# Performance work log

Hardware: AMD Instinct MI355X
Metric: run time of the kernel (lower is better)

Reference implementation:

```python
import jax, jax.numpy as jnp
import numpy as np

L = 9  # local window size


def local_windows(x, l):
    # x: (n, c, h, w) -> (n, c, l*l, h, w): all l*l shifted views (zero-padded),
    # equivalent to F.unfold(x, kernel=(l,l), stride=1, padding=l//2).
    n, c, h, w = x.shape
    pad = l // 2
    xp = jnp.pad(x, ((0, 0), (0, 0), (pad, pad), (pad, pad)))
    views = [xp[:, :, i:i + h, j:j + w] for i in range(l) for j in range(l)]
    return jnp.stack(views, axis=2)


def setup_inputs() -> dict:
    key = jax.random.key(0)
    k1, k2, k3 = jax.random.split(key, 3)
    n, c, h, w = 2, 128, 64, 64
    ft = jax.random.normal(k1, (n, c, h, w), dtype=jnp.float32)
    fk = jax.random.normal(k2, (n, c, h, w), dtype=jnp.float32)
    # 1x1 conv weight shared between key and query projections: (out_c, in_c)
    W = jax.random.normal(k3, (128, 128), dtype=jnp.float32) * (1.0 / np.sqrt(128))
    return {"ft": ft, "fk": fk, "W": W}


def reference(ft, fk, W):
    # 1x1 conv == channel matmul
    key = jnp.einsum('oi,nihw->nohw', W, ft)    # key from frame t
    query = jnp.einsum('oi,nihw->nohw', W, fk)  # query from frame k
    # f_similar(query, key, L): per-pixel query dotted with L*L local keys
    key_win = local_windows(key, L)             # (n, c, L*L, h, w)
    sim = jnp.einsum('nchw,nckhw->nhwk', query, key_win)  # (n, h, w, L*L)
    weight = jax.nn.softmax(sim, axis=-1)
    # f_weighting(ft, weight, L): weighted sum of L*L local raw-ft vectors
    ft_win = local_windows(ft, L)                # (n, c, L*L, h, w)
    out = jnp.einsum('nckhw,nhwk->nchw', ft_win, weight)
    return out
```

## Files before the change

kernel.cpp:

```cpp
#include <hip/hip_runtime.h>
#include <hip/hip_bf16.h>


#define Hh 64
#define Ww 64
#define Cc 128
#define Nn 2
#define KK 81
#define HW (Hh * Ww)
#define CHW (Cc * HW)
#define P_TOT (Nn * HW)

typedef _Float16 h8 __attribute__((ext_vector_type(8)));
typedef _Float16 h4 __attribute__((ext_vector_type(4)));
typedef _Float16 h2 __attribute__((ext_vector_type(2)));

__device__ __forceinline__ void fma4(float4& a, const float4 b, const float s) {
    a.x += b.x * s; a.y += b.y * s; a.z += b.z * s; a.w += b.w * s;
}

__device__ __forceinline__ float dot8(const h8 a, const h8 b, float acc) {
#if __has_builtin(__builtin_amdgcn_fdot2)
    h2 a0 = {a[0], a[1]}, b0 = {b[0], b[1]};
    h2 a1 = {a[2], a[3]}, b1 = {b[2], b[3]};
    h2 a2 = {a[4], a[5]}, b2 = {b[4], b[5]};
    h2 a3 = {a[6], a[7]}, b3 = {b[6], b[7]};
    acc = __builtin_amdgcn_fdot2(a0, b0, acc, false);
    acc = __builtin_amdgcn_fdot2(a1, b1, acc, false);
    acc = __builtin_amdgcn_fdot2(a2, b2, acc, false);
    acc = __builtin_amdgcn_fdot2(a3, b3, acc, false);
#else
#pragma unroll
    for (int i = 0; i < 8; ++i) acc += (float)a[i] * (float)b[i];
#endif
    return acc;
}

__global__ __launch_bounds__(256) void proj_kernel(const float* __restrict__ ft,
                                                   const float* __restrict__ fk,
                                                   const float* __restrict__ Wm,
                                                   _Float16* __restrict__ Qbuf,
                                                   _Float16* __restrict__ Kbuf,
                                                   _Float16* __restrict__ fth) {
    __shared__ __align__(16) float Wl[32 * 132];
    __shared__ __align__(16) float xkl[128 * 36];
    __shared__ __align__(16) float xql[128 * 36];
    const int t = threadIdx.x;
    const int p0 = blockIdx.x * 32;
    const int nn = p0 >> 12;
    const int gbase = nn * CHW + (p0 & 4095);

    for (int e = t; e < 128 * 32; e += 256) {
        const int c = e >> 5, pl = e & 31;
        xkl[c * 36 + pl] = ft[gbase + c * HW + pl];
        xql[c * 36 + pl] = fk[gbase + c * HW + pl];
    }

    const int po = t & 7;
    const int oo = t >> 3;
    float4 accK[4], accQ[4];
#pragma unroll
    for (int i = 0; i < 4; ++i) { accK[i] = make_float4(0,0,0,0); accQ[i] = make_float4(0,0,0,0); }

    for (int ch = 0; ch < 4; ++ch) {
        for (int e = t; e < 128 * 32; e += 256) {
            const int o = e >> 5, ii = e & 31;
            Wl[ii * 132 + o] = Wm[o * 128 + (ch << 5) + ii];
        }
        __syncthreads();
#pragma unroll 4
        for (int ii = 0; ii < 32; ++ii) {
            const int i = (ch << 5) + ii;
            const float4 w4 = *(const float4*)&Wl[ii * 132 + (oo << 2)];
            const float4 k4 = *(const float4*)&xkl[i * 36 + (po << 2)];
            const float4 q4 = *(const float4*)&xql[i * 36 + (po << 2)];
            fma4(accK[0], k4, w4.x); fma4(accK[1], k4, w4.y);
            fma4(accK[2], k4, w4.z); fma4(accK[3], k4, w4.w);
            fma4(accQ[0], q4, w4.x); fma4(accQ[1], q4, w4.y);
            fma4(accQ[2], q4, w4.z); fma4(accQ[3], q4, w4.w);
        }
        __syncthreads();
    }

    const int pbase = p0 + (po << 2);
    const float kr[4][4] = {
        {accK[0].x, accK[1].x, accK[2].x, accK[3].x},
        {accK[0].y, accK[1].y, accK[2].y, accK[3].y},
        {accK[0].z, accK[1].z, accK[2].z, accK[3].z},
        {accK[0].w, accK[1].w, accK[2].w, accK[3].w}};
    const float qr[4][4] = {
        {accQ[0].x, accQ[1].x, accQ[2].x, accQ[3].x},
        {accQ[0].y, accQ[1].y, accQ[2].y, accQ[3].y},
        {accQ[0].z, accQ[1].z, accQ[2].z, accQ[3].z},
        {accQ[0].w, accQ[1].w, accQ[2].w, accQ[3].w}};
#pragma unroll
    for (int pp = 0; pp < 4; ++pp) {
        const size_t base = (size_t)(pbase + pp) * 128 + (oo << 2);
        h4 kv, qv;
#pragma unroll
        for (int j = 0; j < 4; ++j) { kv[j] = (_Float16)kr[pp][j]; qv[j] = (_Float16)qr[pp][j]; }
        *(h4*)&Kbuf[base] = kv;
        *(h4*)&Qbuf[base] = qv;
    }

#pragma unroll
    for (int pp = 0; pp < 4; ++pp) {
        h4 v;
#pragma unroll
        for (int j = 0; j < 4; ++j)
            v[j] = (_Float16)xkl[((oo << 2) + j) * 36 + (po << 2) + pp];
        *(h4*)&fth[(size_t)(pbase + pp) * 128 + (oo << 2)] = v;
    }
}

__global__ __launch_bounds__(256, 4) void sim_weight_kernel(const _Float16* __restrict__ Qbuf,
                                                            const _Float16* __restrict__ Kbuf,
                                                            const _Float16* __restrict__ fth,
                                                            float* __restrict__ out) {
    __shared__ __align__(16) unsigned char smem[40720];
    _Float16* Ksw  = (_Float16*)smem;
    _Float16* Qsw  = (_Float16*)(smem + 36864);
    _Float16* ftl  = (_Float16*)smem;
    _Float16* simb = (_Float16*)(smem + 39168);
    float*    redM = (float*)(smem + 40464);
    float*    redS = (float*)(smem + 40592);

    const int t  = threadIdx.x;
    const int b  = blockIdx.x;
    const int x0 = (b & 7) << 3;
    const int y  = (b >> 3) & 63;
    const int nn = b >> 9;
    const int pg0 = (nn << 12) + (y << 6) + x0;

#pragma unroll 3
    for (int e = t; e < 144 * 16; e += 256) {
        const int v = e >> 4, ci = e & 15;
        const int gx = x0 + (v & 15) - 4;
        const int gy = y + (v >> 4) - 4;
        h8 val = {0, 0, 0, 0, 0, 0, 0, 0};
        if ((unsigned)gx < 64u && (unsigned)gy < 64u)
            val = *(const h8*)&Kbuf[(size_t)((nn << 12) + (gy << 6) + gx) * 128 + (ci << 3)];
        *(h8*)&Ksw[(v << 7) + ((ci ^ (v & 15)) << 3)] = val;
    }
    if (t < 128) {
        const int v = t >> 4, ci = t & 15;
        *(h8*)&Qsw[(v << 7) + ((ci ^ v) << 3)] =
            *(const h8*)&Qbuf[(size_t)(pg0 + v) * 128 + (ci << 3)];
    }
    __syncthreads();

    const int p = t & 7, kb = t >> 3;
    const bool has2 = (kb + 64 < KK);
    const int k0 = kb, k1 = kb + 32, k2 = has2 ? kb + 64 : kb;
    const int v0 = (k0 / 9) * 16 + p + k0 % 9;
    const int v1 = (k1 / 9) * 16 + p + k1 % 9;
    const int v2 = (k2 / 9) * 16 + p + k2 % 9;
    const int b0 = v0 << 7, m0 = v0 & 15;
    const int b1 = v1 << 7, m1 = v1 & 15;
    const int b2 = v2 << 7, m2 = v2 & 15;
    const int bq = p << 7;
    float s0 = 0.f, s1 = 0.f, s2 = 0.f;
#pragma unroll 4
    for (int ci = 0; ci < 16; ++ci) {
        const h8 q8 = *(const h8*)&Qsw[bq + ((ci ^ p) << 3)];
        const h8 kA = *(const h8*)&Ksw[b0 + ((ci ^ m0) << 3)];
        const h8 kB = *(const h8*)&Ksw[b1 + ((ci ^ m1) << 3)];
        const h8 kC = *(const h8*)&Ksw[b2 + ((ci ^ m2) << 3)];
        s0 = dot8(q8, kA, s0);
        s1 = dot8(q8, kB, s1);
        s2 = dot8(q8, kC, s2);
    }
    __syncthreads();

#pragma unroll 3
    for (int e = t; e < 144 * 16; e += 256) {
        const int v = e >> 4, ci = e & 15;
        const int gx = x0 + (v & 15) - 4;
        const int gy = y + (v >> 4) - 4;
        h8 val = {0, 0, 0, 0, 0, 0, 0, 0};
        if ((unsigned)gx < 64u && (unsigned)gy < 64u)
            val = *(const h8*)&fth[(size_t)((nn << 12) + (gy << 6) + gx) * 128 + (ci << 3)];
        *(h8*)&ftl[v * 136 + (ci << 3)] = val;
    }

    float m = fmaxf(s0, s1);
    if (has2) m = fmaxf(m, s2);
#pragma unroll
    for (int off = 8; off <= 32; off <<= 1) m = fmaxf(m, __shfl_xor(m, off));
    if ((t & 56) == 0) redM[((t >> 6) << 3) + p] = m;
    __syncthreads();
    float mm = fmaxf(fmaxf(redM[p], redM[8 + p]), fmaxf(redM[16 + p], redM[24 + p]));
    const float e0 = __expf(s0 - mm);
    const float e1 = __expf(s1 - mm);
    const float e2 = has2 ? __expf(s2 - mm) : 0.f;
    simb[k0 * 8 + p] = (_Float16)e0;
    simb[k1 * 8 + p] = (_Float16)e1;
    if (has2) simb[(kb + 64) * 8 + p] = (_Float16)e2;
    float s = e0 + e1 + e2;
#pragma unroll
    for (int off = 8; off <= 32; off <<= 1) s += __shfl_xor(s, off);
    if ((t & 56) == 0) redS[((t >> 6) << 3) + p] = s;
    __syncthreads();
    const float inv = 1.f / (redS[p] + redS[8 + p] + redS[16 + p] + redS[24 + p]);

    const int cq = t >> 3;
    float4 acc = make_float4(0, 0, 0, 0);
    for (int r = 0; r < 9; ++r) {
        const int rb = ((r << 4) + p) * 136 + (cq << 2);
        const int k9 = r * 9;
#pragma unroll
        for (int dx = 0; dx < 9; ++dx) {
            const float w = (float)simb[(k9 + dx) * 8 + p];
            const h4 f = *(const h4*)&ftl[rb + dx * 136];
            acc.x += (float)f[0] * w;
            acc.y += (float)f[1] * w;
            acc.z += (float)f[2] * w;
            acc.w += (float)f[3] * w;
        }
    }
    const size_t ob = (size_t)((nn * Cc + (cq << 2)) << 12) + (y << 6) + x0 + p;
    out[ob]          = acc.x * inv;
    out[ob + HW]     = acc.y * inv;
    out[ob + 2*HW]   = acc.z * inv;
    out[ob + 3*HW]   = acc.w * inv;
}

extern "C" void kernel_launch(void* const* d_in, const int* in_sizes, int n_in,
                              void* d_out, int out_size, void* d_ws, size_t ws_size,
                              hipStream_t stream) {
    const float* ft = (const float*)d_in[0];
    const float* fk = (const float*)d_in[1];
    const float* Wm = (const float*)d_in[2];
    float* out = (float*)d_out;

    _Float16* wsh  = (_Float16*)d_ws;
    _Float16* Qbuf = wsh;
    _Float16* Kbuf = wsh + 1048576;
    _Float16* fth  = wsh + 2097152;

    proj_kernel<<<256, 256, 0, stream>>>(ft, fk, Wm, Qbuf, Kbuf, fth);
    sim_weight_kernel<<<1024, 256, 0, stream>>>(Qbuf, Kbuf, fth, out);
}
```

Measured before the change: 89.30 us.

## Compute 1x1 projection with fp16 MFMA instead of scalar fp32 FMAs

The projection kernel now converts W and the input tiles to fp16 in shared memory, with pixels as rows and channels contiguous, and computes key and query with 16x16x32 f16 MFMA instructions. Each wave handles one 16-pixel tile of either key or query across all 128 outputs. W is loaded once per block instead of in four chunks, and the fp16 copy of ft is written from the transposed tile. This cuts ALU work in the projection stage. In exchange the inputs are rounded to fp16 before the matmul, and the output stores are 2-byte scattered writes.

After: 80.52 us. -9.8%, faster.

```diff
diff --git a/kernel.cpp b/kernel.cpp
--- a/kernel.cpp
+++ b/kernel.cpp
@@ -14,10 +14,7 @@
 typedef _Float16 h8 __attribute__((ext_vector_type(8)));
 typedef _Float16 h4 __attribute__((ext_vector_type(4)));
 typedef _Float16 h2 __attribute__((ext_vector_type(2)));
-
-__device__ __forceinline__ void fma4(float4& a, const float4 b, const float s) {
-    a.x += b.x * s; a.y += b.y * s; a.z += b.z * s; a.w += b.w * s;
-}
+typedef float f4v __attribute__((ext_vector_type(4)));
 
 __device__ __forceinline__ float dot8(const h8 a, const h8 b, float acc) {
 #if __has_builtin(__builtin_amdgcn_fdot2)
@@ -42,74 +39,73 @@
                                                    _Float16* __restrict__ Qbuf,
                                                    _Float16* __restrict__ Kbuf,
                                                    _Float16* __restrict__ fth) {
-    __shared__ __align__(16) float Wl[32 * 132];
-    __shared__ __align__(16) float xkl[128 * 36];
-    __shared__ __align__(16) float xql[128 * 36];
+    __shared__ __align__(16) _Float16 Wth[128 * 136];
+    __shared__ __align__(16) _Float16 xkh[32 * 136];
+    __shared__ __align__(16) _Float16 xqh[32 * 136];
     const int t = threadIdx.x;
     const int p0 = blockIdx.x * 32;
     const int nn = p0 >> 12;
     const int gbase = nn * CHW + (p0 & 4095);
 
-    for (int e = t; e < 128 * 32; e += 256) {
-        const int c = e >> 5, pl = e & 31;
-        xkl[c * 36 + pl] = ft[gbase + c * HW + pl];
-        xql[c * 36 + pl] = fk[gbase + c * HW + pl];
-    }
-
-    const int po = t & 7;
-    const int oo = t >> 3;
-    float4 accK[4], accQ[4];
-#pragma unroll
-    for (int i = 0; i < 4; ++i) { accK[i] = make_float4(0,0,0,0); accQ[i] = make_float4(0,0,0,0); }
-
-    for (int ch = 0; ch < 4; ++ch) {
-        for (int e = t; e < 128 * 32; e += 256) {
-            const int o = e >> 5, ii = e & 31;
-            Wl[ii * 132 + o] = Wm[o * 128 + (ch << 5) + ii];
-        }
-        __syncthreads();
 #pragma unroll 4
-        for (int ii = 0; ii < 32; ++ii) {
-            const int i = (ch << 5) + ii;
-            const float4 w4 = *(const float4*)&Wl[ii * 132 + (oo << 2)];
-            const float4 k4 = *(const float4*)&xkl[i * 36 + (po << 2)];
-            const float4 q4 = *(const float4*)&xql[i * 36 + (po << 2)];
-            fma4(accK[0], k4, w4.x); fma4(accK[1], k4, w4.y);
-            fma4(accK[2], k4, w4.z); fma4(accK[3], k4, w4.w);
-            fma4(accQ[0], q4, w4.x); fma4(accQ[1], q4, w4.y);
-            fma4(accQ[2], q4, w4.z); fma4(accQ[3], q4, w4.w);
-        }
-        __syncthreads();
-    }
-
-    const int pbase = p0 + (po << 2);
-    const float kr[4][4] = {
-        {accK[0].x, accK[1].x, accK[2].x, accK[3].x},
-        {accK[0].y, accK[1].y, accK[2].y, accK[3].y},
-        {accK[0].z, accK[1].z, accK[2].z, accK[3].z},
-        {accK[0].w, accK[1].w, accK[2].w, accK[3].w}};
-    const float qr[4][4] = {
-        {accQ[0].x, accQ[1].x, accQ[2].x, accQ[3].x},
-        {accQ[0].y, accQ[1].y, accQ[2].y, accQ[3].y},
-        {accQ[0].z, accQ[1].z, accQ[2].z, accQ[3].z},
-        {accQ[0].w, accQ[1].w, accQ[2].w, accQ[3].w}};
-#pragma unroll
-    for (int pp = 0; pp < 4; ++pp) {
-        const size_t base = (size_t)(pbase + pp) * 128 + (oo << 2);
-        h4 kv, qv;
-#pragma unroll
-        for (int j = 0; j < 4; ++j) { kv[j] = (_Float16)kr[pp][j]; qv[j] = (_Float16)qr[pp][j]; }
-        *(h4*)&Kbuf[base] = kv;
-        *(h4*)&Qbuf[base] = qv;
-    }
-
-#pragma unroll
-    for (int pp = 0; pp < 4; ++pp) {
-        h4 v;
-#pragma unroll
-        for (int j = 0; j < 4; ++j)
-            v[j] = (_Float16)xkl[((oo << 2) + j) * 36 + (po << 2) + pp];
-        *(h4*)&fth[(size_t)(pbase + pp) * 128 + (oo << 2)] = v;
+    for (int e = t; e < 4096; e += 256) {
+        const int n = e >> 5, ch = e & 31;
+        const float4 v = *(const float4*)&Wm[n * 128 + (ch << 2)];
+        h4 hv; hv[0] = (_Float16)v.x; hv[1] = (_Float16)v.y;
+               hv[2] = (_Float16)v.z; hv[3] = (_Float16)v.w;
+        *(h4*)&Wth[n * 136 + (ch << 2)] = hv;
+    }
+#pragma unroll 4
+    for (int e = t; e < 1024; e += 256) {
+        const int c = e >> 3, pc = e & 7;
+        const float4 vk = *(const float4*)&ft[gbase + c * HW + (pc << 2)];
+        const float4 vq = *(const float4*)&fk[gbase + c * HW + (pc << 2)];
+        const int px = pc << 2;
+        xkh[(px    ) * 136 + c] = (_Float16)vk.x;
+        xkh[(px + 1) * 136 + c] = (_Float16)vk.y;
+        xkh[(px + 2) * 136 + c] = (_Float16)vk.z;
+        xkh[(px + 3) * 136 + c] = (_Float16)vk.w;
+        xqh[(px    ) * 136 + c] = (_Float16)vq.x;
+        xqh[(px + 1) * 136 + c] = (_Float16)vq.y;
+        xqh[(px + 2) * 136 + c] = (_Float16)vq.z;
+        xqh[(px + 3) * 136 + c] = (_Float16)vq.w;
+    }
+    __syncthreads();
+
+#pragma unroll
+    for (int e = t; e < 512; e += 256) {
+        const int px = e >> 4, cq = e & 15;
+        *(h8*)&fth[(size_t)(p0 + px) * 128 + (cq << 3)] =
+            *(const h8*)&xkh[px * 136 + (cq << 3)];
+    }
+
+    const int lane = t & 63, wv = t >> 6;
+    const int quad = lane >> 4, l15 = lane & 15;
+    const _Float16* xs = (wv >> 1) ? xqh : xkh;
+    _Float16* dst = (wv >> 1) ? Qbuf : Kbuf;
+    const int mt = wv & 1;
+    const int abase = (mt * 16 + l15) * 136 + (quad << 3);
+    const h8 a0 = *(const h8*)&xs[abase];
+    const h8 a1 = *(const h8*)&xs[abase + 32];
+    const h8 a2 = *(const h8*)&xs[abase + 64];
+    const h8 a3 = *(const h8*)&xs[abase + 96];
+#pragma unroll
+    for (int nt = 0; nt < 8; ++nt) {
+        const int bbase = (nt * 16 + l15) * 136 + (quad << 3);
+        const h8 b0 = *(const h8*)&Wth[bbase];
+        const h8 b1 = *(const h8*)&Wth[bbase + 32];
+        const h8 b2 = *(const h8*)&Wth[bbase + 64];
+        const h8 b3 = *(const h8*)&Wth[bbase + 96];
+        f4v acc = {0.f, 0.f, 0.f, 0.f};
+        acc = __builtin_amdgcn_mfma_f32_16x16x32_f16(a0, b0, acc, 0, 0, 0);
+        acc = __builtin_amdgcn_mfma_f32_16x16x32_f16(a1, b1, acc, 0, 0, 0);
+        acc = __builtin_amdgcn_mfma_f32_16x16x32_f16(a2, b2, acc, 0, 0, 0);
+        acc = __builtin_amdgcn_mfma_f32_16x16x32_f16(a3, b3, acc, 0, 0, 0);
+        const int col = nt * 16 + l15;
+        const size_t rb = (size_t)(p0 + mt * 16 + (quad << 2)) * 128 + col;
+#pragma unroll
+        for (int r = 0; r < 4; ++r)
+            dst[rb + (size_t)r * 128] = (_Float16)acc[r];
     }
 }
 
```
